# Kernel tuning notes

Hardware: AMD Instinct MI355X
Metric: run time of the kernel (lower is better)

Reference implementation:

```python
import jax, jax.numpy as jnp
import numpy as np
from jax import lax

LATENT = 512
HIDDEN = 512
VOCAB = 10
SEQ = 6
BATCH = 32768


def setup_inputs() -> dict:
    key = jax.random.key(0)
    ks = jax.random.split(key, 7)
    s_ih = 1.0 / np.sqrt(HIDDEN)
    return {
        "x": jax.random.normal(ks[0], (BATCH, LATENT), dtype=jnp.float32),
        # PyTorch GRU params, gate order (r, z, n)
        "w_ih": jax.random.uniform(ks[1], (3 * HIDDEN, LATENT), jnp.float32, -s_ih, s_ih),
        "w_hh": jax.random.uniform(ks[2], (3 * HIDDEN, HIDDEN), jnp.float32, -s_ih, s_ih),
        "b_ih": jax.random.uniform(ks[3], (3 * HIDDEN,), jnp.float32, -s_ih, s_ih),
        "b_hh": jax.random.uniform(ks[4], (3 * HIDDEN,), jnp.float32, -s_ih, s_ih),
        "w_out": jax.random.uniform(ks[5], (VOCAB, HIDDEN), jnp.float32, -s_ih, s_ih),
        "b_out": jax.random.uniform(ks[6], (VOCAB,), jnp.float32, -s_ih, s_ih),
    }


def reference(x, w_ih, w_hh, b_ih, b_hh, w_out, b_out):
    # Input to the GRU is x repeated at every timestep, so the input-hidden
    # projection is hoisted out of the time loop (computed once).
    gi = x @ w_ih.T + b_ih                      # (B, 3H), constant over time
    gi_r, gi_z, gi_n = jnp.split(gi, 3, axis=-1)

    def step(h, _):
        gh = h @ w_hh.T + b_hh                  # (B, 3H)
        gh_r, gh_z, gh_n = jnp.split(gh, 3, axis=-1)
        r = jax.nn.sigmoid(gi_r + gh_r)
        z = jax.nn.sigmoid(gi_z + gh_z)
        n = jnp.tanh(gi_n + r * gh_n)
        h_new = (1.0 - z) * n + z * h
        return h_new, h_new

    # Initial hidden state is x itself (hidden_dim == latent_dim).
    _, hs = lax.scan(step, x, None, length=SEQ)  # (SEQ, B, H)
    out = jnp.transpose(hs, (1, 0, 2))           # (B, SEQ, H)
    logits = out @ w_out.T + b_out               # (B, SEQ, VOCAB)
    return logits
```

## Files before the change

### kernel.cpp

```cpp
#include <hip/hip_runtime.h>
#include <hip/hip_bf16.h>
#include <stdint.h>


typedef __bf16 bf16_t;
typedef bf16_t bf16x8 __attribute__((ext_vector_type(8)));
typedef bf16_t bf16x4 __attribute__((ext_vector_type(4)));
typedef float  f32x4  __attribute__((ext_vector_type(4)));
typedef float  f32x2  __attribute__((ext_vector_type(2)));

#define THREADS 512
#define BM      64
#define NBLK    512
#define NSTEP   6

#define WIH_OFF 0u
#define WHH_OFF 1572864u
#define WOP_OFF 3145728u
#define GI_OFF  4194304u

static __device__ __forceinline__ float sigm(float v) { return 1.0f / (1.0f + __expf(-v)); }
static __device__ __forceinline__ float tanhf_(float v) {
  v = fminf(fmaxf(v, -12.0f), 12.0f);
  float e = __expf(2.0f * v);
  return 1.0f - 2.0f / (e + 1.0f);
}
static __device__ __forceinline__ f32x4 up4(bf16x4 v) {
  f32x4 o; o[0] = (float)v[0]; o[1] = (float)v[1]; o[2] = (float)v[2]; o[3] = (float)v[3];
  return o;
}
static __device__ __forceinline__ bf16x4 pk4(f32x4 v) {
  bf16x4 o; o[0] = (bf16_t)v[0]; o[1] = (bf16_t)v[1]; o[2] = (bf16_t)v[2]; o[3] = (bf16_t)v[3];
  return o;
}

__global__ void prep_kernel(const float* __restrict__ wih_f, const float* __restrict__ whh_f,
                            const float* __restrict__ wout_f,
                            bf16x8* __restrict__ wihPk, bf16x8* __restrict__ whhPk,
                            bf16x8* __restrict__ wopPk) {
  int c = blockIdx.x * 256 + threadIdx.x;
  int lane = c & 63, l15 = lane & 15, lk = (lane >> 4) & 3;
  if (c < 196608) {
    int cid = (c < 98304) ? c : c - 98304;
    const float* src = (c < 98304) ? wih_f : whh_f;
    bf16x8* dst = (c < 98304) ? wihPk : whhPk;
    int kk = (cid >> 6) & 15;
    int nt = cid >> 10;
    const float* p = src + (size_t)(nt * 16 + l15) * 512 + kk * 32 + lk * 8;
    bf16x8 o;
    #pragma unroll
    for (int i = 0; i < 8; ++i) o[i] = (bf16_t)p[i];
    dst[cid] = o;
  } else if (c < 197632) {
    int cid = c - 196608;
    int kk = cid >> 6;
    bf16x8 o;
    if (l15 < 10) {
      const float* p = wout_f + (size_t)l15 * 512 + kk * 32 + lk * 8;
      #pragma unroll
      for (int i = 0; i < 8; ++i) o[i] = (bf16_t)p[i];
    } else {
      #pragma unroll
      for (int i = 0; i < 8; ++i) o[i] = (bf16_t)0.0f;
    }
    wopPk[cid] = o;
  }
}

__global__ __launch_bounds__(THREADS, 1) void gru_kernel(
    const float* __restrict__ x, const float* __restrict__ b_ih,
    const float* __restrict__ b_hh, const float* __restrict__ b_out,
    const bf16x8* __restrict__ wih, const bf16x8* __restrict__ whh,
    const bf16x8* __restrict__ wop,
    bf16x4* __restrict__ gi, float* __restrict__ out) {
  __shared__ __align__(16) char hlds[2 * BM * 1024];

  const int tid   = (int)threadIdx.x;
  const int lane  = tid & 63;
  const int wq    = tid >> 6;
  const int l15   = lane & 15;
  const int lk    = lane >> 4;
  const int brow0 = (int)blockIdx.x * BM;
  const int swz   = (l15 & 7) << 4;
  const int kbase = (lk * 16) ^ swz;
  const int cbase = (lk * 8) ^ swz;

  char* cur = hlds;
  char* nxt = hlds + BM * 1024;

  #pragma unroll
  for (int it = 0; it < 16; ++it) {
    int f4  = it * THREADS + tid;
    int row = f4 >> 7, c4 = f4 & 127;
    float4 v = ((const float4*)(x + (size_t)(brow0 + row) * 512))[c4];
    bf16x4 h4 = { (bf16_t)v.x, (bf16_t)v.y, (bf16_t)v.z, (bf16_t)v.w };
    *(bf16x4*)(&cur[row * 1024 + ((c4 * 8) ^ ((row & 7) << 4))]) = h4;
  }
  __syncthreads();

  const size_t gibase = (size_t)blockIdx.x * 24576;

  #pragma unroll
  for (int p = 0; p < 4; ++p) {
    const int jt = wq * 4 + p;
    f32x4 acc[3][4];
    #pragma unroll
    for (int g = 0; g < 3; ++g)
      #pragma unroll
      for (int bt = 0; bt < 4; ++bt) acc[g][bt] = (f32x4){0.f, 0.f, 0.f, 0.f};

    #pragma unroll 4
    for (int kk = 0; kk < 16; ++kk) {
      bf16x8 hf[4];
      #pragma unroll
      for (int bt = 0; bt < 4; ++bt)
        hf[bt] = *(const bf16x8*)(&cur[(bt * 16 + l15) * 1024 + ((kk * 64) ^ kbase)]);
      #pragma unroll
      for (int g = 0; g < 3; ++g) {
        bf16x8 wf = wih[((g * 32 + jt) * 16 + kk) * 64 + lane];
        #pragma unroll
        for (int bt = 0; bt < 4; ++bt)
          acc[g][bt] = __builtin_amdgcn_mfma_f32_16x16x32_bf16(wf, hf[bt], acc[g][bt], 0, 0, 0);
      }
    }
    {
      int j = jt * 16 + lk * 4;
      f32x4 b0 = *(const f32x4*)(b_ih + j) + *(const f32x4*)(b_hh + j);
      f32x4 b1 = *(const f32x4*)(b_ih + 512 + j) + *(const f32x4*)(b_hh + 512 + j);
      f32x4 b2 = *(const f32x4*)(b_ih + 1024 + j);
      #pragma unroll
      for (int bt = 0; bt < 4; ++bt) {
        int cb = jt * 12 + bt;
        gi[gibase + ((size_t)(cb + 0) << 6) + lane] = pk4(acc[0][bt] + b0);
        gi[gibase + ((size_t)(cb + 4) << 6) + lane] = pk4(acc[1][bt] + b1);
        gi[gibase + ((size_t)(cb + 8) << 6) + lane] = pk4(acc[2][bt] + b2);
      }
    }
  }

  for (int t = 0; t < NSTEP; ++t) {
    #pragma unroll
    for (int p = 0; p < 4; ++p) {
      const int jt = wq * 4 + p;
      const int cb = jt * 12;

      bf16x4 gpre[3][4];
      #pragma unroll
      for (int g = 0; g < 3; ++g)
        #pragma unroll
        for (int bt = 0; bt < 4; ++bt)
          gpre[g][bt] = gi[gibase + ((size_t)(cb + g * 4 + bt) << 6) + lane];

      f32x4 acc[3][4];
      #pragma unroll
      for (int g = 0; g < 3; ++g)
        #pragma unroll
        for (int bt = 0; bt < 4; ++bt) acc[g][bt] = (f32x4){0.f, 0.f, 0.f, 0.f};

      #pragma unroll 4
      for (int kk = 0; kk < 16; ++kk) {
        bf16x8 hf[4];
        #pragma unroll
        for (int bt = 0; bt < 4; ++bt)
          hf[bt] = *(const bf16x8*)(&cur[(bt * 16 + l15) * 1024 + ((kk * 64) ^ kbase)]);
        #pragma unroll
        for (int g = 0; g < 3; ++g) {
          bf16x8 wf = whh[((g * 32 + jt) * 16 + kk) * 64 + lane];
          #pragma unroll
          for (int bt = 0; bt < 4; ++bt)
            acc[g][bt] = __builtin_amdgcn_mfma_f32_16x16x32_bf16(wf, hf[bt], acc[g][bt], 0, 0, 0);
        }
      }
      {
        int j = jt * 16 + lk * 4;
        f32x4 bn4 = *(const f32x4*)(b_hh + 1024 + j);
        #pragma unroll
        for (int bt = 0; bt < 4; ++bt) {
          f32x4 gr  = up4(gpre[0][bt]);
          f32x4 gz  = up4(gpre[1][bt]);
          f32x4 gn  = up4(gpre[2][bt]);
          f32x4 hov = up4(*(const bf16x4*)(&cur[(bt * 16 + l15) * 1024 +
                                                ((jt * 32) ^ cbase)]));
          f32x4 hv;
          #pragma unroll
          for (int r = 0; r < 4; ++r) {
            float rv = sigm(gr[r] + acc[0][bt][r]);
            float zv = sigm(gz[r] + acc[1][bt][r]);
            float nv = tanhf_(gn[r] + rv * (acc[2][bt][r] + bn4[r]));
            hv[r] = (1.0f - zv) * nv + zv * hov[r];
          }
          *(bf16x4*)(&nxt[(bt * 16 + l15) * 1024 + ((jt * 32) ^ cbase)]) = pk4(hv);
        }
      }
    }
    __syncthreads();

    { char* tmp = cur; cur = nxt; nxt = tmp; }

    if (wq < 4) {
      f32x4 lacc = (f32x4){0.f, 0.f, 0.f, 0.f};
      #pragma unroll 4
      for (int kk = 0; kk < 16; ++kk) {
        bf16x8 hf = *(const bf16x8*)(&cur[(wq * 16 + l15) * 1024 + ((kk * 64) ^ kbase)]);
        bf16x8 wf = wop[kk * 64 + lane];
        lacc = __builtin_amdgcn_mfma_f32_16x16x32_bf16(wf, hf, lacc, 0, 0, 0);
      }
      size_t ob = (size_t)(brow0 + wq * 16 + l15) * 60 + t * 10 + lk * 4;
      if (lk < 2) {
        f32x2 a = { lacc[0] + b_out[lk * 4 + 0], lacc[1] + b_out[lk * 4 + 1] };
        f32x2 b = { lacc[2] + b_out[lk * 4 + 2], lacc[3] + b_out[lk * 4 + 3] };
        *(f32x2*)(out + ob) = a;
        *(f32x2*)(out + ob + 2) = b;
      } else if (lk == 2) {
        f32x2 a = { lacc[0] + b_out[8], lacc[1] + b_out[9] };
        *(f32x2*)(out + ob) = a;
      }
    }
  }
}

extern "C" void kernel_launch(void* const* d_in, const int* in_sizes, int n_in,
                              void* d_out, int out_size, void* d_ws, size_t ws_size,
                              hipStream_t stream) {
  const float* x     = (const float*)d_in[0];
  const float* wih_f = (const float*)d_in[1];
  const float* whh_f = (const float*)d_in[2];
  const float* b_ih  = (const float*)d_in[3];
  const float* b_hh  = (const float*)d_in[4];
  const float* wout  = (const float*)d_in[5];
  const float* b_out = (const float*)d_in[6];

  char* ws = (char*)d_ws;
  bf16x8* wihPk = (bf16x8*)(ws + WIH_OFF);
  bf16x8* whhPk = (bf16x8*)(ws + WHH_OFF);
  bf16x8* wopPk = (bf16x8*)(ws + WOP_OFF);
  bf16x4* gi    = (bf16x4*)(ws + GI_OFF);

  prep_kernel<<<772, 256, 0, stream>>>(wih_f, whh_f, wout, wihPk, whhPk, wopPk);
  gru_kernel<<<NBLK, THREADS, 0, stream>>>(x, b_ih, b_hh, b_out,
                                           wihPk, whhPk, wopPk, gi, (float*)d_out);
}
```

Baseline: 572.7 us.

## Keep GI projections in registers and switch h LDS to padded k-chunk layout

The hoisted input projection (gi) is now kept in registers across all time steps instead of being written to a global workspace and reloaded every step. The hidden-state LDS buffer switches from an XOR-swizzled row-major layout to a k-chunk-major layout padded to 1040 bytes per chunk, which simplifies addressing and aims to avoid bank conflicts. The intent is to remove per-step global traffic for gi. In exchange it costs 48 extra VGPRs of bf16x4 per thread, which raises register pressure and could cause spills at 512 threads per block.

```diff
diff --git a/kernel.cpp b/kernel.cpp
--- a/kernel.cpp
+++ b/kernel.cpp
@@ -13,11 +13,12 @@
 #define BM      64
 #define NBLK    512
 #define NSTEP   6
+#define CH      1040
+#define BUFB    (64 * CH)
 
 #define WIH_OFF 0u
 #define WHH_OFF 1572864u
 #define WOP_OFF 3145728u
-#define GI_OFF  4194304u
 
 static __device__ __forceinline__ float sigm(float v) { return 1.0f / (1.0f + __expf(-v)); }
 static __device__ __forceinline__ float tanhf_(float v) {
@@ -71,9 +72,8 @@
     const float* __restrict__ x, const float* __restrict__ b_ih,
     const float* __restrict__ b_hh, const float* __restrict__ b_out,
     const bf16x8* __restrict__ wih, const bf16x8* __restrict__ whh,
-    const bf16x8* __restrict__ wop,
-    bf16x4* __restrict__ gi, float* __restrict__ out) {
-  __shared__ __align__(16) char hlds[2 * BM * 1024];
+    const bf16x8* __restrict__ wop, float* __restrict__ out) {
+  __shared__ __align__(16) char hlds[2 * BUFB];
 
   const int tid   = (int)threadIdx.x;
   const int lane  = tid & 63;
@@ -81,12 +81,9 @@
   const int l15   = lane & 15;
   const int lk    = lane >> 4;
   const int brow0 = (int)blockIdx.x * BM;
-  const int swz   = (l15 & 7) << 4;
-  const int kbase = (lk * 16) ^ swz;
-  const int cbase = (lk * 8) ^ swz;
 
   char* cur = hlds;
-  char* nxt = hlds + BM * 1024;
+  char* nxt = hlds + BUFB;
 
   #pragma unroll
   for (int it = 0; it < 16; ++it) {
@@ -94,62 +91,55 @@
     int row = f4 >> 7, c4 = f4 & 127;
     float4 v = ((const float4*)(x + (size_t)(brow0 + row) * 512))[c4];
     bf16x4 h4 = { (bf16_t)v.x, (bf16_t)v.y, (bf16_t)v.z, (bf16_t)v.w };
-    *(bf16x4*)(&cur[row * 1024 + ((c4 * 8) ^ ((row & 7) << 4))]) = h4;
+    *(bf16x4*)(&cur[(c4 >> 1) * CH + row * 16 + (c4 & 1) * 8]) = h4;
   }
   __syncthreads();
 
-  const size_t gibase = (size_t)blockIdx.x * 24576;
-
-  #pragma unroll
-  for (int p = 0; p < 4; ++p) {
-    const int jt = wq * 4 + p;
-    f32x4 acc[3][4];
+  bf16x4 gireg[4][3][4];
+
+  {
+    const char* aB = cur + lk * CH + l15 * 16;
     #pragma unroll
-    for (int g = 0; g < 3; ++g)
-      #pragma unroll
-      for (int bt = 0; bt < 4; ++bt) acc[g][bt] = (f32x4){0.f, 0.f, 0.f, 0.f};
-
-    #pragma unroll 4
-    for (int kk = 0; kk < 16; ++kk) {
-      bf16x8 hf[4];
-      #pragma unroll
-      for (int bt = 0; bt < 4; ++bt)
-        hf[bt] = *(const bf16x8*)(&cur[(bt * 16 + l15) * 1024 + ((kk * 64) ^ kbase)]);
-      #pragma unroll
-      for (int g = 0; g < 3; ++g) {
-        bf16x8 wf = wih[((g * 32 + jt) * 16 + kk) * 64 + lane];
+    for (int p = 0; p < 4; ++p) {
+      const int jt = wq * 4 + p;
+      f32x4 acc[3][4];
+      #pragma unroll
+      for (int g = 0; g < 3; ++g)
+        #pragma unroll
+        for (int bt = 0; bt < 4; ++bt) acc[g][bt] = (f32x4){0.f, 0.f, 0.f, 0.f};
+
+      #pragma unroll 4
+      for (int kk = 0; kk < 16; ++kk) {
+        bf16x8 hf[4];
         #pragma unroll
         for (int bt = 0; bt < 4; ++bt)
-          acc[g][bt] = __builtin_amdgcn_mfma_f32_16x16x32_bf16(wf, hf[bt], acc[g][bt], 0, 0, 0);
-      }
-    }
-    {
+          hf[bt] = *(const bf16x8*)(aB + kk * 4160 + bt * 256);
+        #pragma unroll
+        for (int g = 0; g < 3; ++g) {
+          bf16x8 wf = wih[((g * 32 + jt) * 16 + kk) * 64 + lane];
+          #pragma unroll
+          for (int bt = 0; bt < 4; ++bt)
+            acc[g][bt] = __builtin_amdgcn_mfma_f32_16x16x32_bf16(wf, hf[bt], acc[g][bt], 0, 0, 0);
+        }
+      }
       int j = jt * 16 + lk * 4;
       f32x4 b0 = *(const f32x4*)(b_ih + j) + *(const f32x4*)(b_hh + j);
       f32x4 b1 = *(const f32x4*)(b_ih + 512 + j) + *(const f32x4*)(b_hh + 512 + j);
       f32x4 b2 = *(const f32x4*)(b_ih + 1024 + j);
       #pragma unroll
       for (int bt = 0; bt < 4; ++bt) {
-        int cb = jt * 12 + bt;
-        gi[gibase + ((size_t)(cb + 0) << 6) + lane] = pk4(acc[0][bt] + b0);
-        gi[gibase + ((size_t)(cb + 4) << 6) + lane] = pk4(acc[1][bt] + b1);
-        gi[gibase + ((size_t)(cb + 8) << 6) + lane] = pk4(acc[2][bt] + b2);
+        gireg[p][0][bt] = pk4(acc[0][bt] + b0);
+        gireg[p][1][bt] = pk4(acc[1][bt] + b1);
+        gireg[p][2][bt] = pk4(acc[2][bt] + b2);
       }
     }
   }
 
   for (int t = 0; t < NSTEP; ++t) {
+    const char* aB = cur + lk * CH + l15 * 16;
     #pragma unroll
     for (int p = 0; p < 4; ++p) {
       const int jt = wq * 4 + p;
-      const int cb = jt * 12;
-
-      bf16x4 gpre[3][4];
-      #pragma unroll
-      for (int g = 0; g < 3; ++g)
-        #pragma unroll
-        for (int bt = 0; bt < 4; ++bt)
-          gpre[g][bt] = gi[gibase + ((size_t)(cb + g * 4 + bt) << 6) + lane];
 
       f32x4 acc[3][4];
       #pragma unroll
@@ -162,7 +152,7 @@
         bf16x8 hf[4];
         #pragma unroll
         for (int bt = 0; bt < 4; ++bt)
-          hf[bt] = *(const bf16x8*)(&cur[(bt * 16 + l15) * 1024 + ((kk * 64) ^ kbase)]);
+          hf[bt] = *(const bf16x8*)(aB + kk * 4160 + bt * 256);
         #pragma unroll
         for (int g = 0; g < 3; ++g) {
           bf16x8 wf = whh[((g * 32 + jt) * 16 + kk) * 64 + lane];
@@ -174,13 +164,13 @@
       {
         int j = jt * 16 + lk * 4;
         f32x4 bn4 = *(const f32x4*)(b_hh + 1024 + j);
+        const int cof = jt * 2 * CH + (lk >> 1) * CH + l15 * 16 + (lk & 1) * 8;
         #pragma unroll
         for (int bt = 0; bt < 4; ++bt) {
-          f32x4 gr  = up4(gpre[0][bt]);
-          f32x4 gz  = up4(gpre[1][bt]);
-          f32x4 gn  = up4(gpre[2][bt]);
-          f32x4 hov = up4(*(const bf16x4*)(&cur[(bt * 16 + l15) * 1024 +
-                                                ((jt * 32) ^ cbase)]));
+          f32x4 gr  = up4(gireg[p][0][bt]);
+          f32x4 gz  = up4(gireg[p][1][bt]);
+          f32x4 gn  = up4(gireg[p][2][bt]);
+          f32x4 hov = up4(*(const bf16x4*)(cur + cof + bt * 256));
           f32x4 hv;
           #pragma unroll
           for (int r = 0; r < 4; ++r) {
@@ -189,7 +179,7 @@
             float nv = tanhf_(gn[r] + rv * (acc[2][bt][r] + bn4[r]));
             hv[r] = (1.0f - zv) * nv + zv * hov[r];
           }
-          *(bf16x4*)(&nxt[(bt * 16 + l15) * 1024 + ((jt * 32) ^ cbase)]) = pk4(hv);
+          *(bf16x4*)(nxt + cof + bt * 256) = pk4(hv);
         }
       }
     }
@@ -198,10 +188,11 @@
     { char* tmp = cur; cur = nxt; nxt = tmp; }
 
     if (wq < 4) {
+      const char* aL = cur + lk * CH + l15 * 16 + wq * 256;
       f32x4 lacc = (f32x4){0.f, 0.f, 0.f, 0.f};
       #pragma unroll 4
       for (int kk = 0; kk < 16; ++kk) {
-        bf16x8 hf = *(const bf16x8*)(&cur[(wq * 16 + l15) * 1024 + ((kk * 64) ^ kbase)]);
+        bf16x8 hf = *(const bf16x8*)(aL + kk * 4160);
         bf16x8 wf = wop[kk * 64 + lane];
         lacc = __builtin_amdgcn_mfma_f32_16x16x32_bf16(wf, hf, lacc, 0, 0, 0);
       }
@@ -234,9 +225,8 @@
   bf16x8* wihPk = (bf16x8*)(ws + WIH_OFF);
   bf16x8* whhPk = (bf16x8*)(ws + WHH_OFF);
   bf16x8* wopPk = (bf16x8*)(ws + WOP_OFF);
-  bf16x4* gi    = (bf16x4*)(ws + GI_OFF);
 
   prep_kernel<<<772, 256, 0, stream>>>(wih_f, whh_f, wout, wihPk, whhPk, wopPk);
   gru_kernel<<<NBLK, THREADS, 0, stream>>>(x, b_ih, b_hh, b_out,
-                                           wihPk, whhPk, wopPk, gi, (float*)d_out);
-}
+                                           wihPk, whhPk, wopPk, (float*)d_out);
+}
```

Measured after the change: 1.291 ms. 125% more time.

## Retile warp work as 2x4 grid over batch rows and hidden columns

Applied to the files above, without the earlier changes.

Each of the eight waves now covers two 16-row batch tiles and two hidden tiles per pass, where before it covered all four batch tiles and one hidden tile. This halves LDS reads of h per MFMA and doubles the weight fragment loads per wave. Total global weight traffic per block doubles because each weight tile is now loaded by two waves. It trades LDS bandwidth for global/L2 weight bandwidth.

```diff
diff --git a/kernel.cpp b/kernel.cpp
--- a/kernel.cpp
+++ b/kernel.cpp
@@ -78,6 +78,8 @@
   const int tid   = (int)threadIdx.x;
   const int lane  = tid & 63;
   const int wq    = tid >> 6;
+  const int wm    = wq >> 2;
+  const int wn    = wq & 3;
   const int l15   = lane & 15;
   const int lk    = lane >> 4;
   const int brow0 = (int)blockIdx.x * BM;
@@ -102,38 +104,44 @@
 
   #pragma unroll
   for (int p = 0; p < 4; ++p) {
-    const int jt = wq * 4 + p;
-    f32x4 acc[3][4];
-    #pragma unroll
-    for (int g = 0; g < 3; ++g)
-      #pragma unroll
-      for (int bt = 0; bt < 4; ++bt) acc[g][bt] = (f32x4){0.f, 0.f, 0.f, 0.f};
+    const int jt0 = wn * 8 + p * 2;
+    f32x4 acc[2][3][2];
+    #pragma unroll
+    for (int jj = 0; jj < 2; ++jj)
+      #pragma unroll
+      for (int g = 0; g < 3; ++g)
+        #pragma unroll
+        for (int bl = 0; bl < 2; ++bl) acc[jj][g][bl] = (f32x4){0.f, 0.f, 0.f, 0.f};
 
     #pragma unroll 4
     for (int kk = 0; kk < 16; ++kk) {
-      bf16x8 hf[4];
-      #pragma unroll
-      for (int bt = 0; bt < 4; ++bt)
-        hf[bt] = *(const bf16x8*)(&cur[(bt * 16 + l15) * 1024 + ((kk * 64) ^ kbase)]);
-      #pragma unroll
-      for (int g = 0; g < 3; ++g) {
-        bf16x8 wf = wih[((g * 32 + jt) * 16 + kk) * 64 + lane];
-        #pragma unroll
-        for (int bt = 0; bt < 4; ++bt)
-          acc[g][bt] = __builtin_amdgcn_mfma_f32_16x16x32_bf16(wf, hf[bt], acc[g][bt], 0, 0, 0);
-      }
-    }
-    {
+      bf16x8 hf[2];
+      #pragma unroll
+      for (int bl = 0; bl < 2; ++bl)
+        hf[bl] = *(const bf16x8*)(&cur[((wm * 2 + bl) * 16 + l15) * 1024 + ((kk * 64) ^ kbase)]);
+      #pragma unroll
+      for (int jj = 0; jj < 2; ++jj)
+        #pragma unroll
+        for (int g = 0; g < 3; ++g) {
+          bf16x8 wf = wih[((g * 32 + jt0 + jj) * 16 + kk) * 64 + lane];
+          #pragma unroll
+          for (int bl = 0; bl < 2; ++bl)
+            acc[jj][g][bl] = __builtin_amdgcn_mfma_f32_16x16x32_bf16(wf, hf[bl], acc[jj][g][bl], 0, 0, 0);
+        }
+    }
+    #pragma unroll
+    for (int jj = 0; jj < 2; ++jj) {
+      const int jt = jt0 + jj;
       int j = jt * 16 + lk * 4;
       f32x4 b0 = *(const f32x4*)(b_ih + j) + *(const f32x4*)(b_hh + j);
       f32x4 b1 = *(const f32x4*)(b_ih + 512 + j) + *(const f32x4*)(b_hh + 512 + j);
       f32x4 b2 = *(const f32x4*)(b_ih + 1024 + j);
       #pragma unroll
-      for (int bt = 0; bt < 4; ++bt) {
-        int cb = jt * 12 + bt;
-        gi[gibase + ((size_t)(cb + 0) << 6) + lane] = pk4(acc[0][bt] + b0);
-        gi[gibase + ((size_t)(cb + 4) << 6) + lane] = pk4(acc[1][bt] + b1);
-        gi[gibase + ((size_t)(cb + 8) << 6) + lane] = pk4(acc[2][bt] + b2);
+      for (int bl = 0; bl < 2; ++bl) {
+        int bt = wm * 2 + bl;
+        gi[gibase + ((size_t)((jt * 3 + 0) * 4 + bt) << 6) + lane] = pk4(acc[jj][0][bl] + b0);
+        gi[gibase + ((size_t)((jt * 3 + 1) * 4 + bt) << 6) + lane] = pk4(acc[jj][1][bl] + b1);
+        gi[gibase + ((size_t)((jt * 3 + 2) * 4 + bt) << 6) + lane] = pk4(acc[jj][2][bl] + b2);
       }
     }
   }
@@ -141,55 +149,63 @@
   for (int t = 0; t < NSTEP; ++t) {
     #pragma unroll
     for (int p = 0; p < 4; ++p) {
-      const int jt = wq * 4 + p;
-      const int cb = jt * 12;
-
-      bf16x4 gpre[3][4];
-      #pragma unroll
-      for (int g = 0; g < 3; ++g)
-        #pragma unroll
-        for (int bt = 0; bt < 4; ++bt)
-          gpre[g][bt] = gi[gibase + ((size_t)(cb + g * 4 + bt) << 6) + lane];
-
-      f32x4 acc[3][4];
-      #pragma unroll
-      for (int g = 0; g < 3; ++g)
-        #pragma unroll
-        for (int bt = 0; bt < 4; ++bt) acc[g][bt] = (f32x4){0.f, 0.f, 0.f, 0.f};
+      const int jt0 = wn * 8 + p * 2;
+
+      bf16x4 gpre[2][3][2];
+      #pragma unroll
+      for (int jj = 0; jj < 2; ++jj)
+        #pragma unroll
+        for (int g = 0; g < 3; ++g)
+          #pragma unroll
+          for (int bl = 0; bl < 2; ++bl)
+            gpre[jj][g][bl] = gi[gibase +
+                ((size_t)(((jt0 + jj) * 3 + g) * 4 + wm * 2 + bl) << 6) + lane];
+
+      f32x4 acc[2][3][2];
+      #pragma unroll
+      for (int jj = 0; jj < 2; ++jj)
+        #pragma unroll
+        for (int g = 0; g < 3; ++g)
+          #pragma unroll
+          for (int bl = 0; bl < 2; ++bl) acc[jj][g][bl] = (f32x4){0.f, 0.f, 0.f, 0.f};
 
       #pragma unroll 4
       for (int kk = 0; kk < 16; ++kk) {
-        bf16x8 hf[4];
-        #pragma unroll
-        for (int bt = 0; bt < 4; ++bt)
-          hf[bt] = *(const bf16x8*)(&cur[(bt * 16 + l15) * 1024 + ((kk * 64) ^ kbase)]);
-        #pragma unroll
-        for (int g = 0; g < 3; ++g) {
-          bf16x8 wf = whh[((g * 32 + jt) * 16 + kk) * 64 + lane];
-          #pragma unroll
-          for (int bt = 0; bt < 4; ++bt)
-            acc[g][bt] = __builtin_amdgcn_mfma_f32_16x16x32_bf16(wf, hf[bt], acc[g][bt], 0, 0, 0);
-        }
-      }
-      {
+        bf16x8 hf[2];
+        #pragma unroll
+        for (int bl = 0; bl < 2; ++bl)
+          hf[bl] = *(const bf16x8*)(&cur[((wm * 2 + bl) * 16 + l15) * 1024 + ((kk * 64) ^ kbase)]);
+        #pragma unroll
+        for (int jj = 0; jj < 2; ++jj)
+          #pragma unroll
+          for (int g = 0; g < 3; ++g) {
+            bf16x8 wf = whh[((g * 32 + jt0 + jj) * 16 + kk) * 64 + lane];
+            #pragma unroll
+            for (int bl = 0; bl < 2; ++bl)
+              acc[jj][g][bl] = __builtin_amdgcn_mfma_f32_16x16x32_bf16(wf, hf[bl], acc[jj][g][bl], 0, 0, 0);
+          }
+      }
+      #pragma unroll
+      for (int jj = 0; jj < 2; ++jj) {
+        const int jt = jt0 + jj;
         int j = jt * 16 + lk * 4;
         f32x4 bn4 = *(const f32x4*)(b_hh + 1024 + j);
         #pragma unroll
-        for (int bt = 0; bt < 4; ++bt) {
-          f32x4 gr  = up4(gpre[0][bt]);
-          f32x4 gz  = up4(gpre[1][bt]);
-          f32x4 gn  = up4(gpre[2][bt]);
-          f32x4 hov = up4(*(const bf16x4*)(&cur[(bt * 16 + l15) * 1024 +
-                                                ((jt * 32) ^ cbase)]));
+        for (int bl = 0; bl < 2; ++bl) {
+          int row = (wm * 2 + bl) * 16 + l15;
+          f32x4 gr  = up4(gpre[jj][0][bl]);
+          f32x4 gz  = up4(gpre[jj][1][bl]);
+          f32x4 gn  = up4(gpre[jj][2][bl]);
+          f32x4 hov = up4(*(const bf16x4*)(&cur[row * 1024 + ((jt * 32) ^ cbase)]));
           f32x4 hv;
           #pragma unroll
           for (int r = 0; r < 4; ++r) {
-            float rv = sigm(gr[r] + acc[0][bt][r]);
-            float zv = sigm(gz[r] + acc[1][bt][r]);
-            float nv = tanhf_(gn[r] + rv * (acc[2][bt][r] + bn4[r]));
+            float rv = sigm(gr[r] + acc[jj][0][bl][r]);
+            float zv = sigm(gz[r] + acc[jj][1][bl][r]);
+            float nv = tanhf_(gn[r] + rv * (acc[jj][2][bl][r] + bn4[r]));
             hv[r] = (1.0f - zv) * nv + zv * hov[r];
           }
-          *(bf16x4*)(&nxt[(bt * 16 + l15) * 1024 + ((jt * 32) ^ cbase)]) = pk4(hv);
+          *(bf16x4*)(&nxt[row * 1024 + ((jt * 32) ^ cbase)]) = pk4(hv);
         }
       }
     }
```

Result: slower. 1.578 ms (+175.6%).
